# Performance work log

Hardware: AMD Instinct MI355X
Metric: run time of the kernel (lower is better)

Reference implementation:

```python
import jax, jax.numpy as jnp
import numpy as np

B, LQ, LK, D = 64, 1024, 1024, 64
TEMPERATURE = 8.0  # sqrt(D)


def setup_inputs() -> dict:
    key = jax.random.key(0)
    k1, k2, k3, k4, k5, k6 = jax.random.split(key, 6)
    query = jax.random.normal(k1, (B, LQ, D), dtype=jnp.float32)
    key_t = jax.random.normal(k2, (B, LK, D), dtype=jnp.float32)
    value = jax.random.normal(k3, (B, LK, D), dtype=jnp.float32)
    query_mask = jax.random.uniform(k4, (B, LQ)) > 0.1
    key_mask = jax.random.uniform(k5, (B, LK)) > 0.1
    mask = jax.random.uniform(k6, (B, LQ, LK)) > 0.1
    return {"query": query, "key": key_t, "value": value,
            "query_mask": query_mask, "key_mask": key_mask, "mask": mask}


def reference(query, key, value, query_mask, key_mask, mask):
    # unnormalized score: bmm + scale + key/general masking with -inf
    attn = jnp.einsum('bqd,bkd->bqk', query, key) / TEMPERATURE
    neg_inf = jnp.array(-jnp.inf, dtype=attn.dtype)
    if key_mask is not None:
        attn = jnp.where(key_mask[:, None, :], attn, neg_inf)
    if mask is not None:
        attn = jnp.where(mask, attn, neg_inf)
    # softmax over key dim, then zero out masked queries
    attn = jax.nn.softmax(attn, axis=2)
    if query_mask is not None:
        attn = jnp.where(query_mask[:, :, None], attn, 0.0)
    attn_value = jnp.einsum('bqk,bkd->bqd', attn, value)
    return attn_value, attn
```

## Files before the change

kernel.cpp:

```cpp
#include <hip/hip_runtime.h>
#include <hip/hip_bf16.h>


#define NB   64
#define SLQ  1024
#define SLK  1024
#define DH   64
#define TQ   16
#define TK   64
#define NKT  16
#define VSTR 76
#define PSTR 40
#define OSTR 68

typedef __attribute__((ext_vector_type(4))) float          f32x4;
typedef __attribute__((ext_vector_type(8))) __bf16         bf16x8;
typedef __attribute__((ext_vector_type(8))) unsigned short u16x8;
typedef __attribute__((ext_vector_type(4))) unsigned short u16x4;

static __device__ __forceinline__ unsigned short f2bf(float f) {
  return __builtin_bit_cast(unsigned short, (__bf16)f);
}
static __device__ __forceinline__ bf16x8 cvt8(f32x4 a, f32x4 b) {
  bf16x8 r;
#pragma unroll
  for (int i = 0; i < 4; ++i) { r[i] = (__bf16)a[i]; r[i + 4] = (__bf16)b[i]; }
  return r;
}
static __device__ __forceinline__ u16x4 cvt4(f32x4 v) {
  u16x4 h;
#pragma unroll
  for (int i = 0; i < 4; ++i) h[i] = f2bf(v[i]);
  return h;
}

__global__ __launch_bounds__(256, 3) void sdpa_fused(
    const float* __restrict__ Q, const float* __restrict__ K,
    const float* __restrict__ V, const int* __restrict__ QM,
    const int* __restrict__ KM, const int* __restrict__ MSK,
    float* __restrict__ OUT_AV, float* __restrict__ OUT_P) {
  const int g    = blockIdx.x;
  const int slot = g >> 3;
  const int b    = ((slot >> 6) << 3) | (g & 7);
  const int q0   = (slot & 63) * TQ;

  const int tid  = threadIdx.x;
  const int wave = tid >> 6;
  const int lane = tid & 63;
  const int col  = lane & 15;
  const int quad = lane >> 4;
  const int lrow = quad;
  const int lc4  = col * 4;

  __shared__ __align__(16) unsigned char RAW[25216];
  unsigned short* Vw = (unsigned short*)(RAW + wave * (32 * VSTR * 2));
  float*          Ow = (float*)(RAW + wave * (32 * VSTR * 2));
  unsigned short* Pw = (unsigned short*)(RAW + 19456) + wave * (16 * PSTR);
  float* partM = (float*)(RAW + 24576);
  float* partL = partM + 64;
  float* rowM  = partL + 64;
  float* rowS  = rowM + 16;

  const size_t mbase = ((size_t)b * SLQ + q0) * SLK;
  const f32x4* vb4 = (const f32x4*)(V + (size_t)b * SLK * DH);

  const float* qp = Q + ((size_t)b * SLQ + q0 + col) * DH + quad * 8;
  bf16x8 aq0, aq1;
  {
    f32x4 a = *(const f32x4*)qp        * 0.125f;
    f32x4 c = *(const f32x4*)(qp + 4)  * 0.125f;
    f32x4 d = *(const f32x4*)(qp + 32) * 0.125f;
    f32x4 e = *(const f32x4*)(qp + 36) * 0.125f;
    aq0 = cvt8(a, c);
    aq1 = cvt8(d, e);
  }

  const float* kp  = K + ((size_t)b * SLK + wave * 16 + col) * DH + quad * 8;
  const int*   kmp = KM + b * SLK + wave * 16 + col;
  const int*   mkp = MSK + mbase + (size_t)(quad * 4) * SLK + wave * 16 + col;

  float sreg[NKT][4];
#pragma unroll
  for (int kt = 0; kt < NKT; ++kt) {
    const float* kq = kp + (size_t)kt * (TK * DH);
    f32x4 k0 = *(const f32x4*)kq;
    f32x4 k1 = *(const f32x4*)(kq + 4);
    f32x4 k2 = *(const f32x4*)(kq + 32);
    f32x4 k3 = *(const f32x4*)(kq + 36);
    const int km = kmp[kt * TK];
    int mr[4];
#pragma unroll
    for (int r = 0; r < 4; ++r) mr[r] = mkp[(size_t)r * SLK + kt * TK];
    bf16x8 bk0 = cvt8(k0, k1);
    bf16x8 bk1 = cvt8(k2, k3);
    f32x4 acc = {0.f, 0.f, 0.f, 0.f};
    acc = __builtin_amdgcn_mfma_f32_16x16x32_bf16(aq0, bk0, acc, 0, 0, 0);
    acc = __builtin_amdgcn_mfma_f32_16x16x32_bf16(aq1, bk1, acc, 0, 0, 0);
#pragma unroll
    for (int r = 0; r < 4; ++r)
      sreg[kt][r] = (km && mr[r]) ? acc[r] : -INFINITY;
  }

  f32x4 vreg[8];
#pragma unroll
  for (int j = 0; j < 8; ++j)
    vreg[j] = vb4[(size_t)((j >> 2) * TK + wave * 16 + (j & 3) * 4 + lrow) * 16 + col];

  float Mw[4], Cr[4];
#pragma unroll
  for (int r = 0; r < 4; ++r) {
    float m = sreg[0][r];
#pragma unroll
    for (int kt = 1; kt < NKT; ++kt) m = fmaxf(m, sreg[kt][r]);
#pragma unroll
    for (int off = 1; off < 16; off <<= 1) m = fmaxf(m, __shfl_xor(m, off, 64));
    Mw[r] = m;
    const float mc = fmaxf(m, -1e30f);
    float l = 0.f;
#pragma unroll
    for (int kt = 0; kt < NKT; ++kt) {
      float e = __expf(sreg[kt][r] - mc);
      sreg[kt][r] = e;
      l += e;
    }
#pragma unroll
    for (int off = 1; off < 16; off <<= 1) l += __shfl_xor(l, off, 64);
    if (col == 0) {
      partM[wave * 16 + quad * 4 + r] = Mw[r];
      partL[wave * 16 + quad * 4 + r] = l;
    }
  }
  __syncthreads();
  if (tid < TQ) {
    float M = -INFINITY, L = 0.f;
#pragma unroll
    for (int w = 0; w < 4; ++w) {
      float m_ = partM[w * 16 + tid], l_ = partL[w * 16 + tid];
      float mn = fmaxf(M, m_);
      if (mn != -INFINITY) {
        L = L * __expf(M - mn) + l_ * __expf(m_ - mn);
        M = mn;
      }
    }
    rowM[tid] = fmaxf(M, -1e30f);
    rowS[tid] = (QM[b * SLQ + q0 + tid] && L > 0.f) ? (1.f / L) : 0.f;
  }
  __syncthreads();
#pragma unroll
  for (int r = 0; r < 4; ++r)
    Cr[r] = __expf(fmaxf(Mw[r], -1e30f) - rowM[quad * 4 + r]) * rowS[quad * 4 + r];

  float* outp = OUT_P + mbase + (size_t)(quad * 4) * SLK + wave * 16 + col;

  f32x4 acco[4] = {{0.f,0.f,0.f,0.f},{0.f,0.f,0.f,0.f},
                   {0.f,0.f,0.f,0.f},{0.f,0.f,0.f,0.f}};
#pragma unroll
  for (int st = 0; st < 8; ++st) {
    const int kt0 = st * 2, kt1 = kt0 + 1;
#pragma unroll
    for (int j = 0; j < 8; ++j)
      *(u16x4*)&Vw[(j * 4 + lrow) * VSTR + lc4] = cvt4(vreg[j]);

    float p0[4], p1[4];
#pragma unroll
    for (int r = 0; r < 4; ++r) {
      p0[r] = sreg[kt0][r] * Cr[r];
      p1[r] = sreg[kt1][r] * Cr[r];
      Pw[(quad * 4 + r) * PSTR + col]      = f2bf(p0[r]);
      Pw[(quad * 4 + r) * PSTR + 16 + col] = f2bf(p1[r]);
    }
#pragma unroll
    for (int r = 0; r < 4; ++r) {
      outp[(size_t)r * SLK + kt0 * TK] = p0[r];
      outp[(size_t)r * SLK + kt1 * TK] = p1[r];
    }

    if (st < 7) {
#pragma unroll
      for (int j = 0; j < 8; ++j)
        vreg[j] = vb4[(size_t)((st * 2 + 2 + (j >> 2)) * TK + wave * 16 + (j & 3) * 4 + lrow) * 16
                      + col];
    }

    bf16x8 ap = __builtin_bit_cast(bf16x8, *(const u16x8*)&Pw[col * PSTR + quad * 8]);
#pragma unroll
    for (int n0 = 0; n0 < 4; ++n0) {
      u16x8 rv;
#pragma unroll
      for (int j = 0; j < 8; ++j)
        rv[j] = Vw[(quad * 8 + j) * VSTR + n0 * 16 + col];
      acco[n0] = __builtin_amdgcn_mfma_f32_16x16x32_bf16(
          ap, __builtin_bit_cast(bf16x8, rv), acco[n0], 0, 0, 0);
    }
  }

#pragma unroll
  for (int n0 = 0; n0 < 4; ++n0)
#pragma unroll
    for (int r = 0; r < 4; ++r)
      Ow[(quad * 4 + r) * OSTR + n0 * 16 + col] = acco[n0][r];
  __syncthreads();
  {
    const int qq = tid >> 4, dd = (tid & 15) * 4;
    f32x4 s = {0.f, 0.f, 0.f, 0.f};
#pragma unroll
    for (int w = 0; w < 4; ++w) {
      const float* Os = (const float*)(RAW + w * (32 * VSTR * 2));
      s += *(const f32x4*)&Os[(qq & 15) * OSTR + dd + (qq >> 4) * 0];
    }
    *(f32x4*)&OUT_AV[((size_t)b * SLQ + q0 + (qq & 15)) * DH + dd] = s;
  }
}

extern "C" void kernel_launch(void* const* d_in, const int* in_sizes, int n_in,
                              void* d_out, int out_size, void* d_ws, size_t ws_size,
                              hipStream_t stream) {
  const float* q  = (const float*)d_in[0];
  const float* k  = (const float*)d_in[1];
  const float* v  = (const float*)d_in[2];
  const int*   qm = (const int*)d_in[3];
  const int*   km = (const int*)d_in[4];
  const int*   mk = (const int*)d_in[5];
  float* out_av = (float*)d_out;
  float* out_p  = out_av + (size_t)NB * SLQ * DH;
  sdpa_fused<<<dim3(NB * (SLQ / TQ)), dim3(256), 0, stream>>>(q, k, v, qm, km, mk, out_av, out_p);
}
```

Measured before the change: 625.4 us.

## Prefetch K and mask tiles ahead and apply masks after exponentiation

K tiles are now double-buffered in registers and mask values are prefetched eight tiles ahead. This hides global-load latency in the QK^T loop instead of stalling on each tile's loads before its MFMA. Mask results are packed into bitfields and applied as zeroing after the exponential, rather than substituting -inf before the max, which removes the special-case -inf handling in the row combine. The attention-probability stores to global memory are moved out of the PV loop into one pass after it. The costs are higher register pressure at a launch bound of 3 blocks per CU. The row max now includes masked scores, which could in principle underflow the unmasked terms.

```diff
diff --git a/kernel.cpp b/kernel.cpp
--- a/kernel.cpp
+++ b/kernel.cpp
@@ -9,6 +9,7 @@
 #define TQ   16
 #define TK   64
 #define NKT  16
+#define MD   8
 #define VSTR 76
 #define PSTR 40
 #define OSTR 68
@@ -79,26 +80,57 @@
   const int*   kmp = KM + b * SLK + wave * 16 + col;
   const int*   mkp = MSK + mbase + (size_t)(quad * 4) * SLK + wave * 16 + col;
 
+  f32x4 krg[2][4];
+#pragma unroll
+  for (int t = 0; t < 2; ++t) {
+    const float* kq = kp + (size_t)t * (TK * DH);
+    krg[t][0] = *(const f32x4*)kq;
+    krg[t][1] = *(const f32x4*)(kq + 4);
+    krg[t][2] = *(const f32x4*)(kq + 32);
+    krg[t][3] = *(const f32x4*)(kq + 36);
+  }
+  int msq[MD][5];
+#pragma unroll
+  for (int t = 0; t < MD; ++t) {
+    msq[t][0] = kmp[t * TK];
+#pragma unroll
+    for (int r = 0; r < 4; ++r) msq[t][r + 1] = mkp[(size_t)r * SLK + t * TK];
+  }
+
   float sreg[NKT][4];
+  unsigned mbits0 = 0u, mbits1 = 0u;
 #pragma unroll
   for (int kt = 0; kt < NKT; ++kt) {
-    const float* kq = kp + (size_t)kt * (TK * DH);
-    f32x4 k0 = *(const f32x4*)kq;
-    f32x4 k1 = *(const f32x4*)(kq + 4);
-    f32x4 k2 = *(const f32x4*)(kq + 32);
-    f32x4 k3 = *(const f32x4*)(kq + 36);
-    const int km = kmp[kt * TK];
-    int mr[4];
-#pragma unroll
-    for (int r = 0; r < 4; ++r) mr[r] = mkp[(size_t)r * SLK + kt * TK];
-    bf16x8 bk0 = cvt8(k0, k1);
-    bf16x8 bk1 = cvt8(k2, k3);
+    bf16x8 bk0 = cvt8(krg[kt & 1][0], krg[kt & 1][1]);
+    bf16x8 bk1 = cvt8(krg[kt & 1][2], krg[kt & 1][3]);
+    if (kt < NKT - 2) {
+      const float* kq = kp + (size_t)(kt + 2) * (TK * DH);
+      krg[kt & 1][0] = *(const f32x4*)kq;
+      krg[kt & 1][1] = *(const f32x4*)(kq + 4);
+      krg[kt & 1][2] = *(const f32x4*)(kq + 32);
+      krg[kt & 1][3] = *(const f32x4*)(kq + 36);
+    }
     f32x4 acc = {0.f, 0.f, 0.f, 0.f};
     acc = __builtin_amdgcn_mfma_f32_16x16x32_bf16(aq0, bk0, acc, 0, 0, 0);
     acc = __builtin_amdgcn_mfma_f32_16x16x32_bf16(aq1, bk1, acc, 0, 0, 0);
 #pragma unroll
-    for (int r = 0; r < 4; ++r)
-      sreg[kt][r] = (km && mr[r]) ? acc[r] : -INFINITY;
+    for (int r = 0; r < 4; ++r) sreg[kt][r] = acc[r];
+
+    {
+      const int km = msq[kt & (MD - 1)][0];
+      unsigned bits = 0u;
+#pragma unroll
+      for (int r = 0; r < 4; ++r)
+        bits |= (unsigned)(km & msq[kt & (MD - 1)][r + 1] & 1) << r;
+      if (kt < 8) mbits0 |= bits << ((kt & 7) * 4);
+      else        mbits1 |= bits << ((kt & 7) * 4);
+    }
+    if (kt < NKT - MD) {
+      msq[kt & (MD - 1)][0] = kmp[(kt + MD) * TK];
+#pragma unroll
+      for (int r = 0; r < 4; ++r)
+        msq[kt & (MD - 1)][r + 1] = mkp[(size_t)r * SLK + (kt + MD) * TK];
+    }
   }
 
   f32x4 vreg[8];
@@ -115,18 +147,19 @@
 #pragma unroll
     for (int off = 1; off < 16; off <<= 1) m = fmaxf(m, __shfl_xor(m, off, 64));
     Mw[r] = m;
-    const float mc = fmaxf(m, -1e30f);
     float l = 0.f;
 #pragma unroll
     for (int kt = 0; kt < NKT; ++kt) {
-      float e = __expf(sreg[kt][r] - mc);
+      float e = __expf(sreg[kt][r] - m);
+      const unsigned mb = (kt < 8) ? mbits0 : mbits1;
+      e = ((mb >> ((kt & 7) * 4 + r)) & 1u) ? e : 0.f;
       sreg[kt][r] = e;
       l += e;
     }
 #pragma unroll
     for (int off = 1; off < 16; off <<= 1) l += __shfl_xor(l, off, 64);
     if (col == 0) {
-      partM[wave * 16 + quad * 4 + r] = Mw[r];
+      partM[wave * 16 + quad * 4 + r] = m;
       partL[wave * 16 + quad * 4 + r] = l;
     }
   }
@@ -137,20 +170,16 @@
     for (int w = 0; w < 4; ++w) {
       float m_ = partM[w * 16 + tid], l_ = partL[w * 16 + tid];
       float mn = fmaxf(M, m_);
-      if (mn != -INFINITY) {
-        L = L * __expf(M - mn) + l_ * __expf(m_ - mn);
-        M = mn;
-      }
-    }
-    rowM[tid] = fmaxf(M, -1e30f);
+      L = L * __expf(M - mn) + l_ * __expf(m_ - mn);
+      M = mn;
+    }
+    rowM[tid] = M;
     rowS[tid] = (QM[b * SLQ + q0 + tid] && L > 0.f) ? (1.f / L) : 0.f;
   }
   __syncthreads();
 #pragma unroll
   for (int r = 0; r < 4; ++r)
-    Cr[r] = __expf(fmaxf(Mw[r], -1e30f) - rowM[quad * 4 + r]) * rowS[quad * 4 + r];
-
-  float* outp = OUT_P + mbase + (size_t)(quad * 4) * SLK + wave * 16 + col;
+    Cr[r] = __expf(Mw[r] - rowM[quad * 4 + r]) * rowS[quad * 4 + r];
 
   f32x4 acco[4] = {{0.f,0.f,0.f,0.f},{0.f,0.f,0.f,0.f},
                    {0.f,0.f,0.f,0.f},{0.f,0.f,0.f,0.f}};
@@ -161,18 +190,10 @@
     for (int j = 0; j < 8; ++j)
       *(u16x4*)&Vw[(j * 4 + lrow) * VSTR + lc4] = cvt4(vreg[j]);
 
-    float p0[4], p1[4];
 #pragma unroll
     for (int r = 0; r < 4; ++r) {
-      p0[r] = sreg[kt0][r] * Cr[r];
-      p1[r] = sreg[kt1][r] * Cr[r];
-      Pw[(quad * 4 + r) * PSTR + col]      = f2bf(p0[r]);
-      Pw[(quad * 4 + r) * PSTR + 16 + col] = f2bf(p1[r]);
-    }
-#pragma unroll
-    for (int r = 0; r < 4; ++r) {
-      outp[(size_t)r * SLK + kt0 * TK] = p0[r];
-      outp[(size_t)r * SLK + kt1 * TK] = p1[r];
+      Pw[(quad * 4 + r) * PSTR + col]      = f2bf(sreg[kt0][r] * Cr[r]);
+      Pw[(quad * 4 + r) * PSTR + 16 + col] = f2bf(sreg[kt1][r] * Cr[r]);
     }
 
     if (st < 7) {
@@ -193,6 +214,13 @@
           ap, __builtin_bit_cast(bf16x8, rv), acco[n0], 0, 0, 0);
     }
   }
+
+  float* outp = OUT_P + mbase + (size_t)(quad * 4) * SLK + wave * 16 + col;
+#pragma unroll
+  for (int kt = 0; kt < NKT; ++kt)
+#pragma unroll
+    for (int r = 0; r < 4; ++r)
+      outp[(size_t)r * SLK + kt * TK] = sreg[kt][r] * Cr[r];
 
 #pragma unroll
   for (int n0 = 0; n0 < 4; ++n0)
@@ -206,9 +234,9 @@
 #pragma unroll
     for (int w = 0; w < 4; ++w) {
       const float* Os = (const float*)(RAW + w * (32 * VSTR * 2));
-      s += *(const f32x4*)&Os[(qq & 15) * OSTR + dd + (qq >> 4) * 0];
-    }
-    *(f32x4*)&OUT_AV[((size_t)b * SLQ + q0 + (qq & 15)) * DH + dd] = s;
+      s += *(const f32x4*)&Os[qq * OSTR + dd];
+    }
+    *(f32x4*)&OUT_AV[((size_t)b * SLQ + q0 + qq) * DH + dd] = s;
   }
 }
 
```

Result: faster. 610.3 us (-2.4%).
